# Kernel optimization log

Measured on AMD Instinct MI355X. Metric: run time of the kernel, lower is better.

The kernel has to match this reference:

```python
import jax, jax.numpy as jnp
import numpy as np

EPS = 1e-5
ROPE_BASE = 10000.0

def rms_norm(x, w):
    return x * jax.lax.rsqrt(jnp.mean(x * x, axis=-1, keepdims=True) + EPS) * w

def rope_cos_sin(positions, head_dim):
    inv_freq = 1.0 / (ROPE_BASE ** (jnp.arange(0, head_dim, 2, dtype=jnp.float32) / head_dim))
    ang = positions.astype(jnp.float32)[:, None] * inv_freq[None, :]          # [L, hd/2]
    emb = jnp.concatenate([ang, ang], axis=-1)                                # [L, hd]
    return jnp.cos(emb), jnp.sin(emb)

def rotate_half(x):
    d = x.shape[-1] // 2
    return jnp.concatenate([-x[..., d:], x[..., :d]], axis=-1)

def apply_rope(x, cos, sin):
    # x: [B,H,L,hd]; cos/sin: [L,hd]
    return x * cos[None, None] + rotate_half(x) * sin[None, None]

def setup_inputs() -> dict:
    key = jax.random.key(0)
    ks = jax.random.split(key, 12)
    B, S, D = 1, 2048, 2048
    H, KVH, HD = 16, 8, 128
    FF, CACHE = 5632, 2048
    s = 0.02
    return {
        "hidden_states": jax.random.normal(ks[0], (B, S, D), jnp.float32),
        "k_cache": jax.random.normal(ks[1], (B, H, CACHE, HD), jnp.float32),
        "v_cache": jax.random.normal(ks[2], (B, H, CACHE, HD), jnp.float32),
        "q_w": jax.random.normal(ks[3], (H * HD, D), jnp.float32) * s,
        "k_w": jax.random.normal(ks[4], (KVH * HD, D), jnp.float32) * s,
        "v_w": jax.random.normal(ks[5], (KVH * HD, D), jnp.float32) * s,
        "o_w": jax.random.normal(ks[6], (D, H * HD), jnp.float32) * s,
        "gate_w": jax.random.normal(ks[7], (FF, D), jnp.float32) * s,
        "up_w": jax.random.normal(ks[8], (FF, D), jnp.float32) * s,
        "down_w": jax.random.normal(ks[9], (D, FF), jnp.float32) * s,
        "ln1_w": jnp.ones((D,), jnp.float32),
        "ln2_w": jnp.ones((D,), jnp.float32),
        "chunk_size": 512,
    }

def reference(hidden_states, k_cache, v_cache, q_w, k_w, v_w, o_w,
              gate_w, up_w, down_w, ln1_w, ln2_w, chunk_size):
    B, S, D = hidden_states.shape
    H = k_cache.shape[1]
    HD = k_cache.shape[-1]
    KVH = k_w.shape[0] // HD
    group = H // KVH
    prefix = k_cache.shape[2]

    # --- input RMSNorm ---
    residual = hidden_states
    h = rms_norm(hidden_states, ln1_w)

    # --- QKV projections (GQA) ---
    q = (h @ q_w.T).reshape(B, S, H, HD).transpose(0, 2, 1, 3)                # [B,H,S,hd]
    k = (h @ k_w.T).reshape(B, S, KVH, HD).transpose(0, 2, 1, 3)              # [B,KVH,S,hd]
    v = (h @ v_w.T).reshape(B, S, KVH, HD).transpose(0, 2, 1, 3)
    k = jnp.repeat(k, group, axis=1)                                          # repeat_kv -> [B,H,S,hd]
    v = jnp.repeat(v, group, axis=1)

    # --- KV-cache concat along seq ---
    keys = jnp.concatenate([k_cache, k], axis=2)                              # [B,H,P+S,hd]
    vals = jnp.concatenate([v_cache, v], axis=2)
    kv_len = prefix + S

    # --- inline RoPE: keys at 0..kv_len-1, queries at prefix..kv_len-1 ---
    cos_k, sin_k = rope_cos_sin(jnp.arange(kv_len), HD)
    q = apply_rope(q, cos_k[prefix:], sin_k[prefix:])
    keys = apply_rope(keys, cos_k, sin_k)

    # --- hybrid chunked attention mask ---
    # query i (local) sees: full cache prefix + causal positions within its own chunk
    i = jnp.arange(S)
    j = jnp.arange(kv_len)
    local_j = j - prefix
    prefix_vis = (j[None, :] < prefix)
    same_chunk = (i[:, None] // chunk_size) == (local_j[None, :] // chunk_size)
    causal = local_j[None, :] <= i[:, None]
    mask = prefix_vis | (same_chunk & causal)                                 # [S, kv_len]

    scores = jnp.einsum("bhqd,bhkd->bhqk", q, keys) / jnp.sqrt(jnp.float32(HD))
    scores = jnp.where(mask[None, None], scores, jnp.finfo(scores.dtype).min)
    probs = jax.nn.softmax(scores, axis=-1)
    attn = jnp.einsum("bhqk,bhkd->bhqd", probs, vals)                         # [B,H,S,hd]
    attn = attn.transpose(0, 2, 1, 3).reshape(B, S, H * HD) @ o_w.T

    h = residual + attn

    # --- SwiGLU MLP ---
    residual = h
    h = rms_norm(h, ln2_w)
    h = (jax.nn.silu(h @ gate_w.T) * (h @ up_w.T)) @ down_w.T
    return residual + h
```

## Files before the change

### kernel.cpp

```cpp
#include <hip/hip_runtime.h>


#define S_LEN   2048
#define D_MODEL 2048
#define NH      16
#define KVHEADS 8
#define HDIM    128
#define FFDIM   5632
#define PREFIX  2048
#define KVLEN   4096
#define SM_L2E  0.12751744f
#define MCONST  16.0f
#define LN10K_64 0.14391156831212787f

using bf16x8 = __attribute__((ext_vector_type(8))) short;
using f32x4  = __attribute__((ext_vector_type(4))) float;

__device__ __forceinline__ unsigned f2bf_u(float f) {
  unsigned u = __float_as_uint(f);
  return (u + 0x7fffu + ((u >> 16) & 1u)) >> 16;
}
__device__ __forceinline__ unsigned short f2bf(float f) { return (unsigned short)f2bf_u(f); }
__device__ __forceinline__ float bf2f(unsigned short u) {
  return __uint_as_float((unsigned)u << 16);
}
__device__ __forceinline__ unsigned pack2(float a, float b) {
  return f2bf_u(a) | (f2bf_u(b) << 16);
}
__device__ __forceinline__ uint2 pack4(float4 v) {
  uint2 r;
  r.x = pack2(v.x, v.y);
  r.y = pack2(v.z, v.w);
  return r;
}
__device__ __forceinline__ f32x4 mfma16(bf16x8 a, bf16x8 b, f32x4 c) {
  return __builtin_amdgcn_mfma_f32_16x16x32_bf16(a, b, c, 0, 0, 0);
}
__device__ __forceinline__ void gl2lds16(const unsigned short* g, unsigned short* l) {
  __builtin_amdgcn_global_load_lds(
      (__attribute__((address_space(1))) void*)(unsigned short*)g,
      (__attribute__((address_space(3))) void*)l, 16, 0, 0);
}

__device__ __forceinline__ void conv_body(const float* __restrict__ src,
                                          unsigned short* __restrict__ dst,
                                          int bseg, int tid) {
  size_t i = (size_t)bseg * 256 + tid;
  const float4* s4 = (const float4*)src;
  float4 a = s4[2 * i], b = s4[2 * i + 1];
  uint2 lo = pack4(a), hi = pack4(b);
  ((uint4*)dst)[i] = make_uint4(lo.x, lo.y, hi.x, hi.y);
}
__global__ __launch_bounds__(256) void convw_k(const float* __restrict__ src,
                                               unsigned short* __restrict__ dst) {
  conv_body(src, dst, blockIdx.x, threadIdx.x);
}
__global__ __launch_bounds__(256) void conv3_k(const float* __restrict__ q,
                                               const float* __restrict__ k,
                                               const float* __restrict__ v,
                                               unsigned short* __restrict__ dst) {
  int b = blockIdx.x;
  if (b < 2048)      conv_body(q, dst, b, threadIdx.x);
  else if (b < 3072) conv_body(k, dst + (size_t)2048 * 2048, b - 2048, threadIdx.x);
  else               conv_body(v, dst + (size_t)3072 * 2048, b - 3072, threadIdx.x);
}
__global__ __launch_bounds__(256) void conv2_k(const float* __restrict__ g,
                                               const float* __restrict__ u,
                                               unsigned short* __restrict__ wg,
                                               unsigned short* __restrict__ wu) {
  int b = blockIdx.x;
  if (b < 5632) conv_body(g, wg, b, threadIdx.x);
  else          conv_body(u, wu, b - 5632, threadIdx.x);
}

template <bool INBF>
__global__ __launch_bounds__(256) void rmsnorm_k(const void* __restrict__ xin,
                                                 const float* __restrict__ w,
                                                 unsigned short* __restrict__ out) {
  const int row = blockIdx.x, tid = threadIdx.x;
  float v[8];
  if constexpr (INBF) {
    const unsigned short* xr = (const unsigned short*)xin + (size_t)row * D_MODEL;
    uint4 u = ((const uint4*)xr)[tid];
    v[0] = bf2f((unsigned short)(u.x & 0xffff)); v[1] = bf2f((unsigned short)(u.x >> 16));
    v[2] = bf2f((unsigned short)(u.y & 0xffff)); v[3] = bf2f((unsigned short)(u.y >> 16));
    v[4] = bf2f((unsigned short)(u.z & 0xffff)); v[5] = bf2f((unsigned short)(u.z >> 16));
    v[6] = bf2f((unsigned short)(u.w & 0xffff)); v[7] = bf2f((unsigned short)(u.w >> 16));
  } else {
    const float4* xr = (const float4*)((const float*)xin + (size_t)row * D_MODEL);
    float4 a = xr[2 * tid], b = xr[2 * tid + 1];
    v[0] = a.x; v[1] = a.y; v[2] = a.z; v[3] = a.w;
    v[4] = b.x; v[5] = b.y; v[6] = b.z; v[7] = b.w;
  }
  float ss = 0.f;
#pragma unroll
  for (int i = 0; i < 8; i++) ss += v[i] * v[i];
#pragma unroll
  for (int off = 1; off < 64; off <<= 1) ss += __shfl_xor(ss, off);
  __shared__ float red[4];
  if ((tid & 63) == 0) red[tid >> 6] = ss;
  __syncthreads();
  const float sc = rsqrtf((red[0] + red[1] + red[2] + red[3]) * (1.0f / D_MODEL) + 1e-5f);
  const float4* w4 = (const float4*)w;
  float4 wa = w4[2 * tid], wb = w4[2 * tid + 1];
  float4 oa = make_float4(v[0]*sc*wa.x, v[1]*sc*wa.y, v[2]*sc*wa.z, v[3]*sc*wa.w);
  float4 ob = make_float4(v[4]*sc*wb.x, v[5]*sc*wb.y, v[6]*sc*wb.z, v[7]*sc*wb.w);
  uint2 lo = pack4(oa), hi = pack4(ob);
  ((uint4*)(out + (size_t)row * D_MODEL))[tid] = make_uint4(lo.x, lo.y, hi.x, hi.y);
}

template <int BN, int EPI>
__global__ __launch_bounds__(256) void gemm_bf(const unsigned short* __restrict__ A,
                                               const unsigned short* __restrict__ B,
                                               const void* __restrict__ res,
                                               void* __restrict__ C,
                                               int M, int N, int K) {
  constexpr int NI = BN / 32;
  __shared__ __align__(16) unsigned short lA[128 * 32];
  __shared__ __align__(16) unsigned short lB[BN * 32];
  const int tid = threadIdx.x, lane = tid & 63, wave = tid >> 6;
  const int r16 = lane & 15, q4 = lane >> 4;
  const int wm = wave >> 1, wn = wave & 1;
  const int m0 = blockIdx.x * 128, n0 = blockIdx.y * BN;

  const int lr = lane >> 2;
  const int lc = (lane & 3) * 8;
  const unsigned short* gA0 = A + (size_t)(m0 + wave * 16 + lr) * K + lc;
  const unsigned short* gA1 = A + (size_t)(m0 + 64 + wave * 16 + lr) * K + lc;
  unsigned short* lA0 = lA + (wave * 16) * 32;
  unsigned short* lA1 = lA + (64 + wave * 16) * 32;
  const unsigned short* gB0 = B + (size_t)(n0 + wave * 16 + lr) * K + lc;
  const unsigned short* gB1 = B + (size_t)(n0 + 64 + wave * 16 + lr) * K + lc;
  unsigned short* lB0 = lB + (wave * 16) * 32;
  unsigned short* lB1 = lB + (64 + wave * 16) * 32;

  f32x4 acc[4][NI];
#pragma unroll
  for (int i = 0; i < 4; i++)
#pragma unroll
    for (int j = 0; j < NI; j++) acc[i][j] = f32x4{0.f, 0.f, 0.f, 0.f};

  for (int k0 = 0; k0 < K; k0 += 32) {
    gl2lds16(gA0, lA0);
    gl2lds16(gA1, lA1);
    gl2lds16(gB0, lB0);
    if constexpr (BN == 128) gl2lds16(gB1, lB1);
    gA0 += 32; gA1 += 32; gB0 += 32;
    if constexpr (BN == 128) gB1 += 32;
    __syncthreads();
    bf16x8 af[4], bfr[NI];
#pragma unroll
    for (int mi = 0; mi < 4; mi++)
      af[mi] = *(const bf16x8*)&lA[(wm * 64 + mi * 16 + r16) * 32 + q4 * 8];
#pragma unroll
    for (int ni = 0; ni < NI; ni++)
      bfr[ni] = *(const bf16x8*)&lB[(wn * (BN / 2) + ni * 16 + r16) * 32 + q4 * 8];
#pragma unroll
    for (int mi = 0; mi < 4; mi++)
#pragma unroll
      for (int ni = 0; ni < NI; ni++)
        acc[mi][ni] = mfma16(af[mi], bfr[ni], acc[mi][ni]);
    __syncthreads();
  }
#pragma unroll
  for (int mi = 0; mi < 4; mi++)
#pragma unroll
    for (int ni = 0; ni < NI; ni++) {
      int col = n0 + wn * (BN / 2) + ni * 16 + r16;
#pragma unroll
      for (int rr = 0; rr < 4; rr++) {
        int row = m0 + wm * 64 + mi * 16 + q4 * 4 + rr;
        size_t idx = (size_t)row * N + col;
        float v = acc[mi][ni][rr];
        if constexpr (EPI == 0) {
          ((unsigned short*)C)[idx] = f2bf(v);
        } else if constexpr (EPI == 1) {
          ((unsigned short*)C)[idx] = f2bf(v + ((const float*)res)[idx]);
        } else {
          ((float*)C)[idx] = v + bf2f(((const unsigned short*)res)[idx]);
        }
      }
    }
}

__global__ __launch_bounds__(256) void gemm_gateup(const unsigned short* __restrict__ A,
                                                   const unsigned short* __restrict__ Bg,
                                                   const unsigned short* __restrict__ Bu,
                                                   unsigned short* __restrict__ act) {
  __shared__ __align__(16) unsigned short lA[128 * 32];
  __shared__ __align__(16) unsigned short lG[64 * 32];
  __shared__ __align__(16) unsigned short lU[64 * 32];
  const int tid = threadIdx.x, lane = tid & 63, wave = tid >> 6;
  const int r16 = lane & 15, q4 = lane >> 4;
  const int wm = wave >> 1, wn = wave & 1;
  const int m0 = blockIdx.x * 128, n0 = blockIdx.y * 64;
  const int K = D_MODEL;

  const int lr = lane >> 2, lc = (lane & 3) * 8;
  const unsigned short* gA0 = A + (size_t)(m0 + wave * 16 + lr) * K + lc;
  const unsigned short* gA1 = A + (size_t)(m0 + 64 + wave * 16 + lr) * K + lc;
  unsigned short* lA0 = lA + (wave * 16) * 32;
  unsigned short* lA1 = lA + (64 + wave * 16) * 32;
  const unsigned short* gG0 = Bg + (size_t)(n0 + wave * 16 + lr) * K + lc;
  const unsigned short* gU0 = Bu + (size_t)(n0 + wave * 16 + lr) * K + lc;
  unsigned short* lG0 = lG + (wave * 16) * 32;
  unsigned short* lU0 = lU + (wave * 16) * 32;

  f32x4 ag[4][2], au[4][2];
#pragma unroll
  for (int i = 0; i < 4; i++)
#pragma unroll
    for (int j = 0; j < 2; j++) { ag[i][j] = f32x4{0.f,0.f,0.f,0.f}; au[i][j] = f32x4{0.f,0.f,0.f,0.f}; }

  for (int k0 = 0; k0 < K; k0 += 32) {
    gl2lds16(gA0, lA0);
    gl2lds16(gA1, lA1);
    gl2lds16(gG0, lG0);
    gl2lds16(gU0, lU0);
    gA0 += 32; gA1 += 32; gG0 += 32; gU0 += 32;
    __syncthreads();
    bf16x8 af[4], bg2[2], bu2[2];
#pragma unroll
    for (int mi = 0; mi < 4; mi++)
      af[mi] = *(const bf16x8*)&lA[(wm * 64 + mi * 16 + r16) * 32 + q4 * 8];
#pragma unroll
    for (int ni = 0; ni < 2; ni++) {
      int r = (wn * 32 + ni * 16 + r16) * 32 + q4 * 8;
      bg2[ni] = *(const bf16x8*)&lG[r];
      bu2[ni] = *(const bf16x8*)&lU[r];
    }
#pragma unroll
    for (int mi = 0; mi < 4; mi++)
#pragma unroll
      for (int ni = 0; ni < 2; ni++) {
        ag[mi][ni] = mfma16(af[mi], bg2[ni], ag[mi][ni]);
        au[mi][ni] = mfma16(af[mi], bu2[ni], au[mi][ni]);
      }
    __syncthreads();
  }
#pragma unroll
  for (int mi = 0; mi < 4; mi++)
#pragma unroll
    for (int ni = 0; ni < 2; ni++) {
      int col = n0 + wn * 32 + ni * 16 + r16;
#pragma unroll
      for (int rr = 0; rr < 4; rr++) {
        int row = m0 + wm * 64 + mi * 16 + q4 * 4 + rr;
        float g = ag[mi][ni][rr], u = au[mi][ni][rr];
        float sil = g / (1.0f + __expf(-g));
        act[(size_t)row * FFDIM + col] = f2bf(sil * u);
      }
    }
}

__global__ __launch_bounds__(256) void rope_k_k(const float* __restrict__ k_cache,
                                                const unsigned short* __restrict__ qkv,
                                                unsigned short* __restrict__ keys_bf) {
  int idx = blockIdx.x * 256 + threadIdx.x;
  int d = idx & 127, j = (idx >> 7) & 4095, h = idx >> 19;
  int dd = d & 63;
  float inv = __expf(-(float)dd * LN10K_64);
  float ang = (float)j * inv;
  float c = cosf(ang), sn = sinf(ang);
  float x, xr;
  if (j < PREFIX) {
    const float* row = k_cache + ((size_t)h * PREFIX + j) * HDIM;
    x = row[d];
    xr = (d < 64) ? -row[d + 64] : row[d - 64];
  } else {
    const unsigned short* row = qkv + (size_t)(j - PREFIX) * 4096 + 2048 + (h >> 1) * HDIM;
    x = bf2f(row[d]);
    xr = (d < 64) ? -bf2f(row[d + 64]) : bf2f(row[d - 64]);
  }
  keys_bf[idx] = f2bf(x * c + xr * sn);
}

__global__ __launch_bounds__(256) void vtrans_k(const float* __restrict__ v_cache,
                                                const unsigned short* __restrict__ qkv,
                                                unsigned short* __restrict__ vals_t) {
  __shared__ float tile[32][33];
  const int h = blockIdx.z, j0 = blockIdx.x * 32, d0 = blockIdx.y * 32;
  const int t = threadIdx.x;
#pragma unroll
  for (int i = 0; i < 4; i++) {
    int e = i * 256 + t;
    int jj = e >> 5, dd = e & 31;
    float v;
    if (j0 < PREFIX)
      v = v_cache[((size_t)h * PREFIX + j0 + jj) * HDIM + d0 + dd];
    else
      v = bf2f(qkv[(size_t)(j0 - PREFIX + jj) * 4096 + 3072 + (h >> 1) * HDIM + d0 + dd]);
    tile[jj][dd] = v;
  }
  __syncthreads();
#pragma unroll
  for (int i = 0; i < 4; i++) {
    int e = i * 256 + t;
    int dd = e >> 5, jj = e & 31;
    vals_t[((size_t)h * HDIM + d0 + dd) * KVLEN + j0 + jj] = f2bf(tile[jj][dd]);
  }
}

__global__ __launch_bounds__(256) void attn_k(const unsigned short* __restrict__ qkv,
                                              const unsigned short* __restrict__ keys,
                                              const unsigned short* __restrict__ valst,
                                              const int* __restrict__ chunkp,
                                              unsigned short* __restrict__ pO,
                                              float* __restrict__ pl) {
  __shared__ __align__(16) unsigned short lK[64 * 128];
  __shared__ __align__(16) unsigned short lV[128 * 64];
  __shared__ __align__(16) unsigned short lP[4][16 * 64];
  const int h = blockIdx.y, q0 = blockIdx.x * 64, seg = blockIdx.z;
  const int tid = threadIdx.x, wave = tid >> 6, lane = tid & 63;
  const int r16 = lane & 15, q4 = lane >> 4;
  const int chunk = chunkp[0];
  const int sw = (r16 & 7) << 4;

  const int qrow = q0 + wave * 16 + r16;
  const unsigned short* qr = qkv + (size_t)qrow * 4096 + h * HDIM;
  float qx[4][8];
#pragma unroll
  for (int ks = 0; ks < 4; ks++) {
    bf16x8 raw = *(const bf16x8*)(qr + ks * 32 + q4 * 8);
#pragma unroll
    for (int j = 0; j < 8; j++) qx[ks][j] = bf2f((unsigned short)raw[j]);
  }
  const float pos = (float)(PREFIX + qrow);
  bf16x8 qf[4];
#pragma unroll
  for (int ks = 0; ks < 4; ks++)
#pragma unroll
    for (int j = 0; j < 8; j++) {
      int d = ks * 32 + q4 * 8 + j;
      float inv = __expf(-(float)(d & 63) * LN10K_64);
      float ang = pos * inv;
      float c = cosf(ang), sn = sinf(ang);
      float other = qx[ks ^ 2][j];
      float rot = (ks < 2) ? -other : other;
      qf[ks][j] = (short)f2bf(qx[ks][j] * c + rot * sn);
    }

  float lrow[4] = {0.f, 0.f, 0.f, 0.f};
  f32x4 oacc[8];
#pragma unroll
  for (int ni = 0; ni < 8; ni++) oacc[ni] = f32x4{0.f, 0.f, 0.f, 0.f};

  const int irow_base = q0 + wave * 16 + q4 * 4;
  const unsigned short* Kh = keys + (size_t)h * KVLEN * HDIM;
  const unsigned short* Vh = valst + (size_t)h * HDIM * KVLEN;

  const int krow = wave * 4 + (lane >> 4);
  const unsigned short* kSrc = Kh + (size_t)(krow * 4) * HDIM
                               + (((lane & 15) ^ (krow & 7)) * 8);
  unsigned short* kDst = lK + (wave * 4) * 128;
  const int vrow = wave * 8 + (lane >> 3);
  const unsigned short* vSrc = Vh + (size_t)vrow * KVLEN
                               + (((lane & 7) ^ ((lane >> 3) & 7)) * 8);
  unsigned short* vDst = lV + (wave * 8) * 64;

  int kt0, ktN;
  if (seg == 0)      { kt0 = 0;    ktN = 1024; }
  else if (seg == 1) { kt0 = 1024; ktN = 2048; }
  else { int cs = (q0 / chunk) * chunk; kt0 = PREFIX + cs; ktN = PREFIX + q0 + 64; }

  for (int kt = kt0; kt < ktN; kt += 64) {
    const bool domask = (seg == 2) && (kt - PREFIX + 64 > q0);
#pragma unroll
    for (int i = 0; i < 4; i++)
      gl2lds16(kSrc + (size_t)(kt + i) * HDIM, kDst + i * 16 * 128);
#pragma unroll
    for (int i = 0; i < 4; i++)
      gl2lds16(vSrc + (size_t)i * 32 * KVLEN + kt, vDst + i * 32 * 64);
    __syncthreads();
    f32x4 s[4];
#pragma unroll
    for (int j = 0; j < 4; j++) s[j] = f32x4{0.f, 0.f, 0.f, 0.f};
#pragma unroll
    for (int ks = 0; ks < 4; ks++)
#pragma unroll
      for (int j = 0; j < 4; j++) {
        bf16x8 kf = *(const bf16x8*)((const char*)lK + (j * 16 + r16) * 256
                                     + ((ks * 64 + q4 * 16) ^ sw));
        s[j] = mfma16(qf[ks], kf, s[j]);
      }
    const int klb = kt - PREFIX + r16 * 4;
#pragma unroll
    for (int rr = 0; rr < 4; rr++) {
      float e0 = fmaf(s[0][rr], SM_L2E, -MCONST);
      float e1 = fmaf(s[1][rr], SM_L2E, -MCONST);
      float e2 = fmaf(s[2][rr], SM_L2E, -MCONST);
      float e3 = fmaf(s[3][rr], SM_L2E, -MCONST);
      if (domask) {
        int irow = irow_base + rr;
        if (klb     > irow) e0 = -1e30f;
        if (klb + 1 > irow) e1 = -1e30f;
        if (klb + 2 > irow) e2 = -1e30f;
        if (klb + 3 > irow) e3 = -1e30f;
      }
      float p0 = exp2f(e0), p1 = exp2f(e1), p2 = exp2f(e2), p3 = exp2f(e3);
      lrow[rr] += (p0 + p1) + (p2 + p3);
      uint2 pk = make_uint2(pack2(p0, p1), pack2(p2, p3));
      int qrw = q4 * 4 + rr;
      *(uint2*)((char*)lP[wave] + qrw * 128 + ((r16 * 8) ^ ((qrw & 7) << 4))) = pk;
    }
    bf16x8 pf0 = *(const bf16x8*)((const char*)lP[wave] + r16 * 128
                                  + ((q4 * 16) ^ sw));
    bf16x8 pf1 = *(const bf16x8*)((const char*)lP[wave] + r16 * 128
                                  + ((64 + q4 * 16) ^ sw));
#pragma unroll
    for (int ni = 0; ni < 8; ni++) {
      bf16x8 v0 = *(const bf16x8*)((const char*)lV + (ni * 16 + r16) * 128
                                   + ((q4 * 16) ^ sw));
      oacc[ni] = mfma16(pf0, v0, oacc[ni]);
      bf16x8 v1 = *(const bf16x8*)((const char*)lV + (ni * 16 + r16) * 128
                                   + ((64 + q4 * 16) ^ sw));
      oacc[ni] = mfma16(pf1, v1, oacc[ni]);
    }
    __syncthreads();
  }

#pragma unroll
  for (int rr = 0; rr < 4; rr++) {
    lrow[rr] += __shfl_xor(lrow[rr], 1);
    lrow[rr] += __shfl_xor(lrow[rr], 2);
    lrow[rr] += __shfl_xor(lrow[rr], 4);
    lrow[rr] += __shfl_xor(lrow[rr], 8);
  }
  const size_t base = (size_t)(seg * NH + h) * S_LEN;
#pragma unroll
  for (int ni = 0; ni < 8; ni++)
#pragma unroll
    for (int rr = 0; rr < 4; rr++)
      pO[(base + irow_base + rr) * HDIM + ni * 16 + r16] = f2bf(oacc[ni][rr]);
  if (r16 == 0) {
#pragma unroll
    for (int rr = 0; rr < 4; rr++) pl[base + irow_base + rr] = lrow[rr];
  }
}

__global__ __launch_bounds__(256) void attn_combine(const unsigned short* __restrict__ pO,
                                                    const float* __restrict__ pl,
                                                    unsigned short* __restrict__ out) {
  int idx = blockIdx.x * 256 + threadIdx.x;
  int d = idx & 127, hq = idx >> 7;
  const int R = NH * S_LEN;
  float L = pl[hq] + pl[hq + R] + pl[hq + 2 * R];
  float o = bf2f(pO[(size_t)hq * HDIM + d])
          + bf2f(pO[(size_t)(hq + R) * HDIM + d])
          + bf2f(pO[(size_t)(hq + 2 * R) * HDIM + d]);
  int h = hq >> 11, q = hq & 2047;
  out[(size_t)q * D_MODEL + h * HDIM + d] = f2bf(o / L);
}

extern "C" void kernel_launch(void* const* d_in, const int* in_sizes, int n_in,
                              void* d_out, int out_size, void* d_ws, size_t ws_size,
                              hipStream_t stream) {
  (void)in_sizes; (void)n_in; (void)out_size;
  const float* hidden  = (const float*)d_in[0];
  const float* k_cache = (const float*)d_in[1];
  const float* v_cache = (const float*)d_in[2];
  const float* q_w     = (const float*)d_in[3];
  const float* k_w     = (const float*)d_in[4];
  const float* v_w     = (const float*)d_in[5];
  const float* o_w     = (const float*)d_in[6];
  const float* gate_w  = (const float*)d_in[7];
  const float* up_w    = (const float*)d_in[8];
  const float* down_w  = (const float*)d_in[9];
  const float* ln1     = (const float*)d_in[10];
  const float* ln2     = (const float*)d_in[11];
  const int*   chunkp  = (const int*)d_in[12];

  if (ws_size < 92274688) return;
  char* ws = (char*)d_ws;
  const size_t MB = 1048576;
  unsigned short* qkvpre = (unsigned short*)(ws + 0 * MB);
  unsigned short* keysbf = (unsigned short*)(ws + 16 * MB);
  unsigned short* valst  = (unsigned short*)(ws + 32 * MB);
  unsigned short* pO     = (unsigned short*)(ws + 48 * MB);
  float*          pl     = (float*)(ws + 88 * MB - 393216);
  unsigned short* WQKV   = (unsigned short*)(ws + 72 * MB);
  unsigned short* hn     = (unsigned short*)(ws + 48 * MB);
  unsigned short* attnbf = (unsigned short*)(ws + 72 * MB);
  unsigned short* WO     = (unsigned short*)(ws + 80 * MB);
  unsigned short* h2     = (unsigned short*)(ws + 48 * MB);
  unsigned short* h2n    = (unsigned short*)(ws + 56 * MB);
  unsigned short* WG     = (unsigned short*)(ws + 0 * MB);
  unsigned short* WU     = (unsigned short*)(ws + 22 * MB);
  unsigned short* act    = (unsigned short*)(ws + 64 * MB);
  unsigned short* WD     = (unsigned short*)(ws + 0 * MB);
  float* out = (float*)d_out;

  rmsnorm_k<false><<<S_LEN, 256, 0, stream>>>(hidden, ln1, hn);
  conv3_k<<<4096, 256, 0, stream>>>(q_w, k_w, v_w, WQKV);
  gemm_bf<128, 0><<<dim3(16, 32), 256, 0, stream>>>(hn, WQKV, nullptr, qkvpre,
                                                    S_LEN, 4096, D_MODEL);
  rope_k_k<<<(NH * KVLEN * HDIM) / 256, 256, 0, stream>>>(k_cache, qkvpre, keysbf);
  vtrans_k<<<dim3(KVLEN / 32, HDIM / 32, NH), 256, 0, stream>>>(v_cache, qkvpre, valst);
  attn_k<<<dim3(S_LEN / 64, NH, 3), 256, 0, stream>>>(qkvpre, keysbf, valst,
                                                      chunkp, pO, pl);
  attn_combine<<<(NH * S_LEN * HDIM) / 256, 256, 0, stream>>>(pO, pl, attnbf);
  convw_k<<<2048, 256, 0, stream>>>(o_w, WO);
  gemm_bf<64, 1><<<dim3(16, 32), 256, 0, stream>>>(attnbf, WO, hidden, h2,
                                                   S_LEN, D_MODEL, D_MODEL);
  rmsnorm_k<true><<<S_LEN, 256, 0, stream>>>(h2, ln2, h2n);
  conv2_k<<<11264, 256, 0, stream>>>(gate_w, up_w, WG, WU);
  gemm_gateup<<<dim3(16, FFDIM / 64), 256, 0, stream>>>(h2n, WG, WU, act);
  convw_k<<<5632, 256, 0, stream>>>(down_w, WD);
  gemm_bf<64, 2><<<dim3(16, 32), 256, 0, stream>>>(act, WD, h2, out,
                                                   S_LEN, D_MODEL, FFDIM);
}
```

Measured before the change: 702.4 us.

## Double-buffer LDS tiles in GEMM and attention kernels to overlap loads

New measurement: 737.9 us. 1.05x slower.

```diff
diff --git a/kernel.cpp b/kernel.cpp
--- a/kernel.cpp
+++ b/kernel.cpp
@@ -116,8 +116,9 @@
                                                void* __restrict__ C,
                                                int M, int N, int K) {
   constexpr int NI = BN / 32;
-  __shared__ __align__(16) unsigned short lA[128 * 32];
-  __shared__ __align__(16) unsigned short lB[BN * 32];
+  constexpr int ASZ = 128 * 32, BSZ = BN * 32;
+  __shared__ __align__(16) unsigned short lA[2 * ASZ];
+  __shared__ __align__(16) unsigned short lB[2 * BSZ];
   const int tid = threadIdx.x, lane = tid & 63, wave = tid >> 6;
   const int r16 = lane & 15, q4 = lane >> 4;
   const int wm = wave >> 1, wn = wave & 1;
@@ -140,27 +141,40 @@
 #pragma unroll
     for (int j = 0; j < NI; j++) acc[i][j] = f32x4{0.f, 0.f, 0.f, 0.f};
 
+  gl2lds16(gA0, lA0);
+  gl2lds16(gA1, lA1);
+  gl2lds16(gB0, lB0);
+  if constexpr (BN == 128) gl2lds16(gB1, lB1);
+  gA0 += 32; gA1 += 32; gB0 += 32;
+  if constexpr (BN == 128) gB1 += 32;
+  __syncthreads();
+
+  int bs = 0;
   for (int k0 = 0; k0 < K; k0 += 32) {
-    gl2lds16(gA0, lA0);
-    gl2lds16(gA1, lA1);
-    gl2lds16(gB0, lB0);
-    if constexpr (BN == 128) gl2lds16(gB1, lB1);
-    gA0 += 32; gA1 += 32; gB0 += 32;
-    if constexpr (BN == 128) gB1 += 32;
-    __syncthreads();
+    if (k0 + 32 < K) {
+      const int ao = (bs ^ 1) * ASZ, bo = (bs ^ 1) * BSZ;
+      gl2lds16(gA0, lA0 + ao);
+      gl2lds16(gA1, lA1 + ao);
+      gl2lds16(gB0, lB0 + bo);
+      if constexpr (BN == 128) gl2lds16(gB1, lB1 + bo);
+      gA0 += 32; gA1 += 32; gB0 += 32;
+      if constexpr (BN == 128) gB1 += 32;
+    }
+    const int ar = bs * ASZ, br = bs * BSZ;
     bf16x8 af[4], bfr[NI];
 #pragma unroll
     for (int mi = 0; mi < 4; mi++)
-      af[mi] = *(const bf16x8*)&lA[(wm * 64 + mi * 16 + r16) * 32 + q4 * 8];
+      af[mi] = *(const bf16x8*)&lA[ar + (wm * 64 + mi * 16 + r16) * 32 + q4 * 8];
 #pragma unroll
     for (int ni = 0; ni < NI; ni++)
-      bfr[ni] = *(const bf16x8*)&lB[(wn * (BN / 2) + ni * 16 + r16) * 32 + q4 * 8];
+      bfr[ni] = *(const bf16x8*)&lB[br + (wn * (BN / 2) + ni * 16 + r16) * 32 + q4 * 8];
 #pragma unroll
     for (int mi = 0; mi < 4; mi++)
 #pragma unroll
       for (int ni = 0; ni < NI; ni++)
         acc[mi][ni] = mfma16(af[mi], bfr[ni], acc[mi][ni]);
     __syncthreads();
+    bs ^= 1;
   }
 #pragma unroll
   for (int mi = 0; mi < 4; mi++)
@@ -187,9 +201,10 @@
                                                    const unsigned short* __restrict__ Bg,
                                                    const unsigned short* __restrict__ Bu,
                                                    unsigned short* __restrict__ act) {
-  __shared__ __align__(16) unsigned short lA[128 * 32];
-  __shared__ __align__(16) unsigned short lG[64 * 32];
-  __shared__ __align__(16) unsigned short lU[64 * 32];
+  constexpr int ASZ = 128 * 32, GSZ = 64 * 32;
+  __shared__ __align__(16) unsigned short lA[2 * ASZ];
+  __shared__ __align__(16) unsigned short lG[2 * GSZ];
+  __shared__ __align__(16) unsigned short lU[2 * GSZ];
   const int tid = threadIdx.x, lane = tid & 63, wave = tid >> 6;
   const int r16 = lane & 15, q4 = lane >> 4;
   const int wm = wave >> 1, wn = wave & 1;
@@ -212,20 +227,31 @@
 #pragma unroll
     for (int j = 0; j < 2; j++) { ag[i][j] = f32x4{0.f,0.f,0.f,0.f}; au[i][j] = f32x4{0.f,0.f,0.f,0.f}; }
 
+  gl2lds16(gA0, lA0);
+  gl2lds16(gA1, lA1);
+  gl2lds16(gG0, lG0);
+  gl2lds16(gU0, lU0);
+  gA0 += 32; gA1 += 32; gG0 += 32; gU0 += 32;
+  __syncthreads();
+
+  int bs = 0;
   for (int k0 = 0; k0 < K; k0 += 32) {
-    gl2lds16(gA0, lA0);
-    gl2lds16(gA1, lA1);
-    gl2lds16(gG0, lG0);
-    gl2lds16(gU0, lU0);
-    gA0 += 32; gA1 += 32; gG0 += 32; gU0 += 32;
-    __syncthreads();
+    if (k0 + 32 < K) {
+      const int ao = (bs ^ 1) * ASZ, go = (bs ^ 1) * GSZ;
+      gl2lds16(gA0, lA0 + ao);
+      gl2lds16(gA1, lA1 + ao);
+      gl2lds16(gG0, lG0 + go);
+      gl2lds16(gU0, lU0 + go);
+      gA0 += 32; gA1 += 32; gG0 += 32; gU0 += 32;
+    }
+    const int ar = bs * ASZ, gr = bs * GSZ;
     bf16x8 af[4], bg2[2], bu2[2];
 #pragma unroll
     for (int mi = 0; mi < 4; mi++)
-      af[mi] = *(const bf16x8*)&lA[(wm * 64 + mi * 16 + r16) * 32 + q4 * 8];
+      af[mi] = *(const bf16x8*)&lA[ar + (wm * 64 + mi * 16 + r16) * 32 + q4 * 8];
 #pragma unroll
     for (int ni = 0; ni < 2; ni++) {
-      int r = (wn * 32 + ni * 16 + r16) * 32 + q4 * 8;
+      int r = gr + (wn * 32 + ni * 16 + r16) * 32 + q4 * 8;
       bg2[ni] = *(const bf16x8*)&lG[r];
       bu2[ni] = *(const bf16x8*)&lU[r];
     }
@@ -237,6 +263,7 @@
         au[mi][ni] = mfma16(af[mi], bu2[ni], au[mi][ni]);
       }
     __syncthreads();
+    bs ^= 1;
   }
 #pragma unroll
   for (int mi = 0; mi < 4; mi++)
@@ -307,14 +334,40 @@
                                               const int* __restrict__ chunkp,
                                               unsigned short* __restrict__ pO,
                                               float* __restrict__ pl) {
-  __shared__ __align__(16) unsigned short lK[64 * 128];
-  __shared__ __align__(16) unsigned short lV[128 * 64];
+  constexpr int KSZ = 64 * 128;
+  constexpr int VSZ = 128 * 64;
+  __shared__ __align__(16) unsigned short lK[2 * KSZ];
+  __shared__ __align__(16) unsigned short lV[2 * VSZ];
   __shared__ __align__(16) unsigned short lP[4][16 * 64];
   const int h = blockIdx.y, q0 = blockIdx.x * 64, seg = blockIdx.z;
   const int tid = threadIdx.x, wave = tid >> 6, lane = tid & 63;
   const int r16 = lane & 15, q4 = lane >> 4;
   const int chunk = chunkp[0];
   const int sw = (r16 & 7) << 4;
+
+  const unsigned short* Kh = keys + (size_t)h * KVLEN * HDIM;
+  const unsigned short* Vh = valst + (size_t)h * HDIM * KVLEN;
+
+  const int krow = wave * 4 + (lane >> 4);
+  const unsigned short* kSrc = Kh + (size_t)(krow * 4) * HDIM
+                               + (((lane & 15) ^ (krow & 7)) * 8);
+  unsigned short* kDst = lK + (wave * 4) * 128;
+  const int vrow = wave * 8 + (lane >> 3);
+  const unsigned short* vSrc = Vh + (size_t)vrow * KVLEN
+                               + (((lane & 7) ^ ((lane >> 3) & 7)) * 8);
+  unsigned short* vDst = lV + (wave * 8) * 64;
+
+  int kt0, ktN;
+  if (seg == 0)      { kt0 = 0;    ktN = 1024; }
+  else if (seg == 1) { kt0 = 1024; ktN = 2048; }
+  else { int cs = (q0 / chunk) * chunk; kt0 = PREFIX + cs; ktN = PREFIX + q0 + 64; }
+
+#pragma unroll
+  for (int i = 0; i < 4; i++)
+    gl2lds16(kSrc + (size_t)(kt0 + i) * HDIM, kDst + i * 16 * 128);
+#pragma unroll
+  for (int i = 0; i < 4; i++)
+    gl2lds16(vSrc + (size_t)i * 32 * KVLEN + kt0, vDst + i * 32 * 64);
 
   const int qrow = q0 + wave * 16 + r16;
   const unsigned short* qr = qkv + (size_t)qrow * 4096 + h * HDIM;
@@ -346,32 +399,23 @@
   for (int ni = 0; ni < 8; ni++) oacc[ni] = f32x4{0.f, 0.f, 0.f, 0.f};
 
   const int irow_base = q0 + wave * 16 + q4 * 4;
-  const unsigned short* Kh = keys + (size_t)h * KVLEN * HDIM;
-  const unsigned short* Vh = valst + (size_t)h * HDIM * KVLEN;
-
-  const int krow = wave * 4 + (lane >> 4);
-  const unsigned short* kSrc = Kh + (size_t)(krow * 4) * HDIM
-                               + (((lane & 15) ^ (krow & 7)) * 8);
-  unsigned short* kDst = lK + (wave * 4) * 128;
-  const int vrow = wave * 8 + (lane >> 3);
-  const unsigned short* vSrc = Vh + (size_t)vrow * KVLEN
-                               + (((lane & 7) ^ ((lane >> 3) & 7)) * 8);
-  unsigned short* vDst = lV + (wave * 8) * 64;
-
-  int kt0, ktN;
-  if (seg == 0)      { kt0 = 0;    ktN = 1024; }
-  else if (seg == 1) { kt0 = 1024; ktN = 2048; }
-  else { int cs = (q0 / chunk) * chunk; kt0 = PREFIX + cs; ktN = PREFIX + q0 + 64; }
-
+
+  __syncthreads();
+
+  int bs = 0;
   for (int kt = kt0; kt < ktN; kt += 64) {
+    if (kt + 64 < ktN) {
+      const int ko = (bs ^ 1) * KSZ, vo = (bs ^ 1) * VSZ;
+#pragma unroll
+      for (int i = 0; i < 4; i++)
+        gl2lds16(kSrc + (size_t)(kt + 64 + i) * HDIM, kDst + ko + i * 16 * 128);
+#pragma unroll
+      for (int i = 0; i < 4; i++)
+        gl2lds16(vSrc + (size_t)i * 32 * KVLEN + kt + 64, vDst + vo + i * 32 * 64);
+    }
     const bool domask = (seg == 2) && (kt - PREFIX + 64 > q0);
-#pragma unroll
-    for (int i = 0; i < 4; i++)
-      gl2lds16(kSrc + (size_t)(kt + i) * HDIM, kDst + i * 16 * 128);
-#pragma unroll
-    for (int i = 0; i < 4; i++)
-      gl2lds16(vSrc + (size_t)i * 32 * KVLEN + kt, vDst + i * 32 * 64);
-    __syncthreads();
+    const char* lKc = (const char*)lK + bs * (KSZ * 2);
+    const char* lVc = (const char*)lV + bs * (VSZ * 2);
     f32x4 s[4];
 #pragma unroll
     for (int j = 0; j < 4; j++) s[j] = f32x4{0.f, 0.f, 0.f, 0.f};
@@ -379,7 +423,7 @@
     for (int ks = 0; ks < 4; ks++)
 #pragma unroll
       for (int j = 0; j < 4; j++) {
-        bf16x8 kf = *(const bf16x8*)((const char*)lK + (j * 16 + r16) * 256
+        bf16x8 kf = *(const bf16x8*)(lKc + (j * 16 + r16) * 256
                                      + ((ks * 64 + q4 * 16) ^ sw));
         s[j] = mfma16(qf[ks], kf, s[j]);
       }
@@ -409,14 +453,15 @@
                                   + ((64 + q4 * 16) ^ sw));
 #pragma unroll
     for (int ni = 0; ni < 8; ni++) {
-      bf16x8 v0 = *(const bf16x8*)((const char*)lV + (ni * 16 + r16) * 128
+      bf16x8 v0 = *(const bf16x8*)(lVc + (ni * 16 + r16) * 128
                                    + ((q4 * 16) ^ sw));
       oacc[ni] = mfma16(pf0, v0, oacc[ni]);
-      bf16x8 v1 = *(const bf16x8*)((const char*)lV + (ni * 16 + r16) * 128
+      bf16x8 v1 = *(const bf16x8*)(lVc + (ni * 16 + r16) * 128
                                    + ((64 + q4 * 16) ^ sw));
       oacc[ni] = mfma16(pf1, v1, oacc[ni]);
     }
     __syncthreads();
+    bs ^= 1;
   }
 
 #pragma unroll
```
